# Optimization experiments

Hardware: AMD Instinct MI355X
Metric: run time of the kernel (lower is better)

The kernel has to match this reference:

```python
import jax, jax.numpy as jnp
import numpy as np

B, N, C_IN, C_OUT, H = 8, 1024, 256, 512, 8
DH = C_OUT // H  # per-head dim
LN_EPS = 1e-5


def setup_inputs() -> dict:
    key = jax.random.key(0)
    ks = jax.random.split(key, 8)
    # xavier_normal std for [in, out] fan pair
    std = float(np.sqrt(2.0 / (C_IN + DH)))
    x = jax.random.normal(ks[0], (B, N, C_IN), dtype=jnp.float32)
    adj = jax.random.uniform(ks[1], (B, N, N), dtype=jnp.float32)
    W_q = jax.random.normal(ks[2], (H, C_IN, DH), dtype=jnp.float32) * std
    W_k = jax.random.normal(ks[3], (H, C_IN, DH), dtype=jnp.float32) * std
    W_v = jax.random.normal(ks[4], (H, C_IN, DH), dtype=jnp.float32) * std
    # Conv1d(in, out, kernel=1) == pointwise linear: weight [out, in], bias [out]
    bound = float(1.0 / np.sqrt(C_IN))
    conv_w = jax.random.uniform(ks[5], (C_OUT, C_IN), dtype=jnp.float32, minval=-bound, maxval=bound)
    conv_b = jax.random.uniform(ks[6], (C_OUT,), dtype=jnp.float32, minval=-bound, maxval=bound)
    ln_w = jnp.ones((C_OUT,), dtype=jnp.float32)
    ln_b = jnp.zeros((C_OUT,), dtype=jnp.float32)
    return {"x": x, "adj": adj, "W_q": W_q, "W_k": W_k, "W_v": W_v,
            "conv_w": conv_w, "conv_b": conv_b, "ln_w": ln_w, "ln_b": ln_b}


def reference(x, adj, W_q, W_k, W_v, conv_w, conv_b, ln_w, ln_b):
    # NOTE: in the original module, adj is used only to compute D_neg/A_hat,
    # which are discarded; it has no effect on the output. Attention is dense.
    dh = W_q.shape[-1]
    scale = 1.0 / jnp.sqrt(jnp.asarray(dh, dtype=x.dtype))
    # batched per-head projections: [B,N,Cin] x [H,Cin,dh] -> [B,H,N,dh]
    Q = jnp.einsum('bni,hio->bhno', x, W_q)
    K = jnp.einsum('bni,hio->bhno', x, W_k)
    V = jnp.einsum('bni,hio->bhno', x, W_v)
    scores = jnp.einsum('bhqd,bhkd->bhqk', Q, K) * scale  # [B,H,N,N]
    attn = jax.nn.softmax(scores, axis=-1)
    out = jax.nn.relu(jnp.einsum('bhqk,bhkd->bhqd', attn, V))  # [B,H,N,dh]
    b, h, n, d = out.shape
    out = out.transpose(0, 2, 1, 3).reshape(b, n, h * d)  # concat heads -> [B,N,Cout]
    # matching_conv: 1x1 conv == linear over channels
    proj = jnp.einsum('bni,oi->bno', x, conv_w) + conv_b
    y = out + proj
    mean = jnp.mean(y, axis=-1, keepdims=True)
    var = jnp.var(y, axis=-1, keepdims=True)
    y = (y - mean) * jax.lax.rsqrt(var + LN_EPS)
    return y * ln_w + ln_b
```

## Files before the change

### kernel.cpp

```cpp
#include <hip/hip_runtime.h>

#define B_ 8
#define N_ 1024
#define CIN_ 256
#define COUT_ 512
#define H_ 8
#define DH_ 64

typedef __attribute__((ext_vector_type(8))) short bf8;
typedef __attribute__((ext_vector_type(4))) short s4;
typedef __attribute__((ext_vector_type(4))) float f4;
typedef __attribute__((ext_vector_type(2))) unsigned int u2;

__device__ __forceinline__ short f2bf(float f) {
  unsigned u = __builtin_bit_cast(unsigned, f);
  u += 0x7fffu + ((u >> 16) & 1u);
  return (short)(u >> 16);
}
__device__ __forceinline__ float bf2f(short s) {
  unsigned u = ((unsigned)(unsigned short)s) << 16;
  return __builtin_bit_cast(float, u);
}

#if __has_builtin(__builtin_amdgcn_exp2f)
#define EXP2 __builtin_amdgcn_exp2f
#else
#define EXP2 exp2f
#endif

__device__ __forceinline__ unsigned cvtpk(float a, float b) {
  unsigned u;
  asm("v_cvt_pk_bf16_f32 %0, %1, %2" : "=v"(u) : "v"(a), "v"(b));
  return u;
}

#define MFMA16(a, b, c) __builtin_amdgcn_mfma_f32_16x16x32_bf16((a), (b), (c), 0, 0, 0)

#define MFMAPV(a, b, c) __builtin_amdgcn_mfma_f32_16x16x16bf16_1k((a), (b), (c), 0, 0, 0)

#define GLD16(gp, lp)                                                              \
  __builtin_amdgcn_global_load_lds((const __attribute__((address_space(1))) void*)(gp), \
                                   (__attribute__((address_space(3))) void*)(lp), 16, 0, 0)

__global__ void k_prep(const float* __restrict__ Wq, const float* __restrict__ Wk,
                       const float* __restrict__ Wv, const float* __restrict__ Cw,
                       const float* __restrict__ x, short* __restrict__ Wt,
                       short* __restrict__ xb) {
  int blk = blockIdx.x;
  if (blk < 2048) {
    int col = blk;
    int k = threadIdx.x;
    float v;
    if (col < 512) {
      int h = col >> 6, d = col & 63;
      v = Wq[(h * CIN_ + k) * DH_ + d];
    } else if (col < 1024) {
      int c = col - 512, h = c >> 6, d = c & 63;
      v = Wk[(h * CIN_ + k) * DH_ + d];
    } else if (col < 1536) {
      int c = col - 1024, h = c >> 6, d = c & 63;
      v = Wv[(h * CIN_ + k) * DH_ + d];
    } else {
      v = Cw[(col - 1536) * CIN_ + k];
    }
    Wt[col * CIN_ + k] = f2bf(v);
  } else {
    int i = (blk - 2048) * 256 + threadIdx.x;
    f4 a = *reinterpret_cast<const f4*>(x + (size_t)i * 8);
    f4 b = *reinterpret_cast<const f4*>(x + (size_t)i * 8 + 4);
    bf8 o;
    o[0] = f2bf(a[0]); o[1] = f2bf(a[1]); o[2] = f2bf(a[2]); o[3] = f2bf(a[3]);
    o[4] = f2bf(b[0]); o[5] = f2bf(b[1]); o[6] = f2bf(b[2]); o[7] = f2bf(b[3]);
    *reinterpret_cast<bf8*>(xb + (size_t)i * 8) = o;
  }
}

__global__ __launch_bounds__(256) void k_gemm(const short* __restrict__ xb, const short* __restrict__ Wt,
                                              short* __restrict__ Qw, short* __restrict__ Kw,
                                              short* __restrict__ Vt, short* __restrict__ Pj) {
  __shared__ short Al[2][128][64];
  __shared__ short Bl[2][128][64];
  int tid = threadIdx.x;
  int mt = blockIdx.x >> 4, nt = blockIdx.x & 15;
  int row0 = mt * 128, col0 = nt * 128;
  int w = tid >> 6, lane = tid & 63, g = lane >> 4, lr = lane & 15;
  int wm = w >> 1, wn = w & 1;
  f4 acc[4][4];
#pragma unroll
  for (int i = 0; i < 4; ++i)
#pragma unroll
    for (int j = 0; j < 4; ++j) acc[i][j] = (f4){0.f, 0.f, 0.f, 0.f};

  int srow[4], sgc[4];
#pragma unroll
  for (int p = 0; p < 4; ++p) {
    int s = p * 256 + tid;
    srow[p] = s >> 3;
    sgc[p] = (s & 7) ^ (srow[p] & 7);
  }

#define STAGE_AB(k0_, buf_)                                                     \
  {                                                                             \
    char* abase = (char*)&Al[buf_][0][0];                                       \
    char* bbase = (char*)&Bl[buf_][0][0];                                       \
    _Pragma("unroll")                                                           \
    for (int p = 0; p < 4; ++p) {                                               \
      int lb = (p * 256 + w * 64) << 4;                                         \
      GLD16(xb + (row0 + srow[p]) * CIN_ + (k0_) + sgc[p] * 8, abase + lb);     \
      GLD16(Wt + (col0 + srow[p]) * CIN_ + (k0_) + sgc[p] * 8, bbase + lb);     \
    }                                                                           \
  }

  STAGE_AB(0, 0);

  for (int kt = 0; kt < 4; ++kt) {
    int cur = kt & 1;
    if (kt < 3) {
      STAGE_AB((kt + 1) * 64, cur ^ 1);
      asm volatile("s_waitcnt vmcnt(8)" ::: "memory");
    } else {
      asm volatile("s_waitcnt vmcnt(0)" ::: "memory");
    }
    __builtin_amdgcn_s_barrier();

    const short* al = &Al[cur][0][0];
    const short* bl = &Bl[cur][0][0];
    bf8 af[4][2], bb[4][2];
#pragma unroll
    for (int mi = 0; mi < 4; ++mi) {
      int R = wm * 64 + mi * 16 + lr;
      int sw = R & 7;
      af[mi][0] = *reinterpret_cast<const bf8*>(al + R * 64 + ((g ^ sw) * 8));
      af[mi][1] = *reinterpret_cast<const bf8*>(al + R * 64 + (((4 + g) ^ sw) * 8));
    }
#pragma unroll
    for (int ni = 0; ni < 4; ++ni) {
      int R = wn * 64 + ni * 16 + lr;
      int sw = R & 7;
      bb[ni][0] = *reinterpret_cast<const bf8*>(bl + R * 64 + ((g ^ sw) * 8));
      bb[ni][1] = *reinterpret_cast<const bf8*>(bl + R * 64 + (((4 + g) ^ sw) * 8));
    }
#pragma unroll
    for (int mi = 0; mi < 4; ++mi)
#pragma unroll
      for (int ni = 0; ni < 4; ++ni) {
        acc[mi][ni] = MFMA16(af[mi][0], bb[ni][0], acc[mi][ni]);
        acc[mi][ni] = MFMA16(af[mi][1], bb[ni][1], acc[mi][ni]);
      }
    asm volatile("s_waitcnt lgkmcnt(0)" ::: "memory");
    __builtin_amdgcn_s_barrier();
  }

  const float QSCL = 0.125f * 1.4426950408889634f;
#pragma unroll
  for (int mi = 0; mi < 4; ++mi)
#pragma unroll
    for (int ni = 0; ni < 4; ++ni) {
      int c = col0 + wn * 64 + ni * 16 + lr;
      int r0 = row0 + wm * 64 + mi * 16 + g * 4;
      int b = r0 >> 10, n0 = r0 & 1023;
      if (c < 1024) {
#pragma unroll
        for (int j = 0; j < 4; ++j) {
          int n = n0 + j;
          if (c < 512) {
            Qw[((b * H_ + (c >> 6)) * N_ + n) * DH_ + (c & 63)] = f2bf(acc[mi][ni][j] * QSCL);
          } else {
            int cc = c - 512;
            Kw[((b * H_ + (cc >> 6)) * N_ + n) * DH_ + (cc & 63)] = f2bf(acc[mi][ni][j]);
          }
        }
      } else if (c < 1536) {
        int cc = c - 1024;
        int hh = cc >> 6, d = cc & 63;
        s4 vv;
#pragma unroll
        for (int j = 0; j < 4; ++j) vv[j] = f2bf(acc[mi][ni][j]);
        *reinterpret_cast<s4*>(Vt + ((size_t)(b * H_ + hh) * DH_ + d) * N_ + n0) = vv;
      } else {
#pragma unroll
        for (int j = 0; j < 4; ++j) {
          Pj[(size_t)(r0 + j) * COUT_ + (c - 1536)] = f2bf(acc[mi][ni][j]);
        }
      }
    }
}

__global__ __launch_bounds__(256) void k_attn(const short* __restrict__ Qw, const short* __restrict__ Kw,
                                              const short* __restrict__ Vt, short* __restrict__ At) {
  __shared__ short Kl[4][64][64];
  __shared__ short Vl[4][64][64];
  int tid = threadIdx.x;
  int nid = ((blockIdx.x & 7) << 6) | (blockIdx.x >> 3);
  int bh = nid >> 3;
  int qb = nid & 7;
  int w = tid >> 6, lane = tid & 63, g = lane >> 4, lr = lane & 15;
  int qglob = qb * 128 + w * 32;
  const short* Qp = Qw + ((size_t)bh * N_ + qglob) * DH_;
  const short* Kp = Kw + (size_t)bh * N_ * DH_;
  const short* Vp = Vt + (size_t)bh * DH_ * N_;

  int sr0 = tid >> 3, sc0 = (tid & 7) ^ (sr0 & 7);
  int s1 = tid + 256;
  int sr1 = s1 >> 3, sc1 = (s1 & 7) ^ (sr1 & 7);
  int lo0 = (w * 64) << 4;
  int lo1 = (w * 64 + 256) << 4;

#define STAGE_KV(tt_, buf_)                                                     \
  {                                                                             \
    const short* kb = Kp + (tt_) * (64 * DH_);                                  \
    const short* vb = Vp + (tt_) * 64;                                          \
    char* klb = (char*)&Kl[buf_][0][0];                                         \
    char* vlb = (char*)&Vl[buf_][0][0];                                         \
    GLD16(kb + sr0 * 64 + sc0 * 8, klb + lo0);                                  \
    GLD16(kb + sr1 * 64 + sc1 * 8, klb + lo1);                                  \
    GLD16(vb + (size_t)sr0 * N_ + sc0 * 8, vlb + lo0);                          \
    GLD16(vb + (size_t)sr1 * N_ + sc1 * 8, vlb + lo1);                          \
  }

  STAGE_KV(0, 0);
  STAGE_KV(1, 1);

  bf8 aq[2][2];
#pragma unroll
  for (int qs = 0; qs < 2; ++qs) {
    aq[qs][0] = *reinterpret_cast<const bf8*>(Qp + (qs * 16 + lr) * DH_ + g * 8);
    aq[qs][1] = *reinterpret_cast<const bf8*>(Qp + (qs * 16 + lr) * DH_ + 32 + g * 8);
  }

  f4 o[2][4];
  f4 lacc[2];
#pragma unroll
  for (int qs = 0; qs < 2; ++qs) {
    lacc[qs] = (f4){0.f, 0.f, 0.f, 0.f};
#pragma unroll
    for (int i = 0; i < 4; ++i) o[qs][i] = (f4){0.f, 0.f, 0.f, 0.f};
  }

  for (int t = 0; t < 16; ++t) {
    int cur = t & 3;
    if (t < 14) {
      STAGE_KV(t + 2, (t + 2) & 3);
      asm volatile("s_waitcnt vmcnt(8)" ::: "memory");
    } else if (t == 14) {
      asm volatile("s_waitcnt vmcnt(4)" ::: "memory");
    } else {
      asm volatile("s_waitcnt vmcnt(0)" ::: "memory");
    }
    __builtin_amdgcn_s_barrier();

    const short* klc = &Kl[cur][0][0];
    bf8 bk0[4], bk1[4];
#pragma unroll
    for (int kt = 0; kt < 4; ++kt) {
      int R = kt * 16 + lr;
      const short* kr = klc + R * 64;
      int sw = (R & 7) << 3;
      bk0[kt] = *reinterpret_cast<const bf8*>(kr + ((g * 8) ^ sw));
      bk1[kt] = *reinterpret_cast<const bf8*>(kr + ((32 + g * 8) ^ sw));
    }
    f4 s0[4], s1v[4];
    __builtin_amdgcn_s_setprio(1);
#pragma unroll
    for (int kt = 0; kt < 4; ++kt) {
      f4 z = (f4){0.f, 0.f, 0.f, 0.f};
      z = MFMA16(bk0[kt], aq[0][0], z);
      z = MFMA16(bk1[kt], aq[0][1], z);
      s0[kt] = z;
      f4 z2 = (f4){0.f, 0.f, 0.f, 0.f};
      z2 = MFMA16(bk0[kt], aq[1][0], z2);
      z2 = MFMA16(bk1[kt], aq[1][1], z2);
      s1v[kt] = z2;
    }
    __builtin_amdgcn_s_setprio(0);
    s4 pq0[4], pq1[4];
#pragma unroll
    for (int kt = 0; kt < 4; ++kt) {
      f4 p;
      p[0] = EXP2(s0[kt][0]); p[1] = EXP2(s0[kt][1]);
      p[2] = EXP2(s0[kt][2]); p[3] = EXP2(s0[kt][3]);
      lacc[0] += p;
      u2 pk;
      pk[0] = cvtpk(p[0], p[1]);
      pk[1] = cvtpk(p[2], p[3]);
      pq0[kt] = __builtin_bit_cast(s4, pk);
    }
#pragma unroll
    for (int kt = 0; kt < 4; ++kt) {
      f4 p;
      p[0] = EXP2(s1v[kt][0]); p[1] = EXP2(s1v[kt][1]);
      p[2] = EXP2(s1v[kt][2]); p[3] = EXP2(s1v[kt][3]);
      lacc[1] += p;
      u2 pk;
      pk[0] = cvtpk(p[0], p[1]);
      pk[1] = cvtpk(p[2], p[3]);
      pq1[kt] = __builtin_bit_cast(s4, pk);
    }

    const short* vlc = &Vl[cur][0][0];
#pragma unroll
    for (int dt = 0; dt < 4; ++dt) {
      int R = dt * 16 + lr;
      const short* vr = vlc + R * 64;
      int swR = R & 7;
      s4 va[4];
#pragma unroll
      for (int kt = 0; kt < 4; ++kt) {
        int ch = (kt * 2 + (g >> 1)) ^ swR;
        va[kt] = *reinterpret_cast<const s4*>(vr + ch * 8 + (g & 1) * 4);
      }
      __builtin_amdgcn_s_setprio(1);
#pragma unroll
      for (int kt = 0; kt < 4; ++kt) {
        o[0][dt] = MFMAPV(va[kt], pq0[kt], o[0][dt]);
        o[1][dt] = MFMAPV(va[kt], pq1[kt], o[1][dt]);
      }
      __builtin_amdgcn_s_setprio(0);
    }
    asm volatile("s_waitcnt lgkmcnt(0)" ::: "memory");
  }

  float ls[2];
#pragma unroll
  for (int qs = 0; qs < 2; ++qs) {
    float v = (lacc[qs][0] + lacc[qs][1]) + (lacc[qs][2] + lacc[qs][3]);
    v += __shfl_xor(v, 16, 64);
    v += __shfl_xor(v, 32, 64);
    ls[qs] = v;
  }
  int b = bh >> 3, h = bh & 7;
#pragma unroll
  for (int qs = 0; qs < 2; ++qs) {
    float inv = 1.f / ls[qs];
    int n = qglob + qs * 16 + lr;
    short* dst = At + ((size_t)b * N_ + n) * COUT_ + h * DH_;
#pragma unroll
    for (int dt = 0; dt < 4; ++dt) {
      s4 ov;
#pragma unroll
      for (int j = 0; j < 4; ++j) ov[j] = f2bf(fmaxf(o[qs][dt][j] * inv, 0.f));
      *reinterpret_cast<s4*>(dst + dt * 16 + g * 4) = ov;
    }
  }
}

__global__ __launch_bounds__(256) void k_ln(const short* __restrict__ At, const short* __restrict__ Pj,
                                            const float* __restrict__ cb, const float* __restrict__ lw,
                                            const float* __restrict__ lb, float* __restrict__ out) {
  int row = blockIdx.x * 4 + (threadIdx.x >> 6);
  int lane = threadIdx.x & 63;
  int c0 = lane * 8;
  bf8 a8 = *reinterpret_cast<const bf8*>(At + (size_t)row * COUT_ + c0);
  bf8 p8 = *reinterpret_cast<const bf8*>(Pj + (size_t)row * COUT_ + c0);
  float y[8];
  float sum = 0.f, sq = 0.f;
#pragma unroll
  for (int j = 0; j < 8; ++j) {
    float v = bf2f(a8[j]) + bf2f(p8[j]) + cb[c0 + j];
    y[j] = v;
    sum += v;
    sq += v * v;
  }
#pragma unroll
  for (int off = 1; off < 64; off <<= 1) {
    sum += __shfl_xor(sum, off, 64);
    sq += __shfl_xor(sq, off, 64);
  }
  float mean = sum * (1.f / 512.f);
  float var = sq * (1.f / 512.f) - mean * mean;
  float rstd = rsqrtf(var + 1e-5f);
  f4 o0, o1;
#pragma unroll
  for (int j = 0; j < 4; ++j) o0[j] = (y[j] - mean) * rstd * lw[c0 + j] + lb[c0 + j];
#pragma unroll
  for (int j = 0; j < 4; ++j) o1[j] = (y[4 + j] - mean) * rstd * lw[c0 + 4 + j] + lb[c0 + 4 + j];
  *reinterpret_cast<f4*>(out + (size_t)row * COUT_ + c0) = o0;
  *reinterpret_cast<f4*>(out + (size_t)row * COUT_ + c0 + 4) = o1;
}

extern "C" void kernel_launch(void* const* d_in, const int* in_sizes, int n_in,
                              void* d_out, int out_size, void* d_ws, size_t ws_size,
                              hipStream_t stream) {
  const float* x  = (const float*)d_in[0];
  const float* Wq = (const float*)d_in[2];
  const float* Wk = (const float*)d_in[3];
  const float* Wv = (const float*)d_in[4];
  const float* Cw = (const float*)d_in[5];
  const float* cb = (const float*)d_in[6];
  const float* lw = (const float*)d_in[7];
  const float* lb = (const float*)d_in[8];
  float* out = (float*)d_out;
  char* ws = (char*)d_ws;
  short* xb = (short*)(ws);
  short* Wt = (short*)(ws + (size_t)4194304);
  short* Qw = (short*)(ws + (size_t)5242880);
  short* Kw = (short*)(ws + (size_t)13631488);
  short* Vt = (short*)(ws + (size_t)22020096);
  short* Pj = (short*)(ws + (size_t)30408704);
  short* At = (short*)(ws + (size_t)38797312);

  hipLaunchKernelGGL(k_prep, dim3(3072), dim3(256), 0, stream, Wq, Wk, Wv, Cw, x, Wt, xb);
  hipLaunchKernelGGL(k_gemm, dim3(1024), dim3(256), 0, stream, xb, Wt, Qw, Kw, Vt, Pj);
  hipLaunchKernelGGL(k_attn, dim3(512), dim3(256), 0, stream, Qw, Kw, Vt, At);
  hipLaunchKernelGGL(k_ln, dim3(2048), dim3(256), 0, stream, At, Pj, cb, lw, lb, out);
}
```

Baseline: 66.40 us.

## Store Q transposed and fold projection residual add into attention epilogue

The GEMM epilogue now writes Q in a head-dim-major transposed layout with vectorized 4-element stores, like V, instead of scattered scalar stores. The attention kernel gathers Q with strided scalar loads before staging K/V. It also adds the bf16 projection result into the attention output before storing it. The layernorm kernel then reads only one bf16 tensor instead of two. The change cuts GEMM store scatter and LN read traffic, but adds uncoalesced Q loads in attention and an extra rounding of the summed value to bf16.

```diff
diff --git a/kernel.cpp b/kernel.cpp
--- a/kernel.cpp
+++ b/kernel.cpp
@@ -35,7 +35,6 @@
 }
 
 #define MFMA16(a, b, c) __builtin_amdgcn_mfma_f32_16x16x32_bf16((a), (b), (c), 0, 0, 0)
-
 #define MFMAPV(a, b, c) __builtin_amdgcn_mfma_f32_16x16x16bf16_1k((a), (b), (c), 0, 0, 0)
 
 #define GLD16(gp, lp)                                                              \
@@ -76,7 +75,7 @@
 }
 
 __global__ __launch_bounds__(256) void k_gemm(const short* __restrict__ xb, const short* __restrict__ Wt,
-                                              short* __restrict__ Qw, short* __restrict__ Kw,
+                                              short* __restrict__ Qt, short* __restrict__ Kw,
                                               short* __restrict__ Vt, short* __restrict__ Pj) {
   __shared__ short Al[2][128][64];
   __shared__ short Bl[2][128][64];
@@ -159,16 +158,18 @@
       int c = col0 + wn * 64 + ni * 16 + lr;
       int r0 = row0 + wm * 64 + mi * 16 + g * 4;
       int b = r0 >> 10, n0 = r0 & 1023;
-      if (c < 1024) {
+      if (c < 512) {
+        int hh = c >> 6, d = c & 63;
+        s4 vv;
+#pragma unroll
+        for (int j = 0; j < 4; ++j) vv[j] = f2bf(acc[mi][ni][j] * QSCL);
+        *reinterpret_cast<s4*>(Qt + ((size_t)(b * H_ + hh) * DH_ + d) * N_ + n0) = vv;
+      } else if (c < 1024) {
+        int cc = c - 512;
 #pragma unroll
         for (int j = 0; j < 4; ++j) {
           int n = n0 + j;
-          if (c < 512) {
-            Qw[((b * H_ + (c >> 6)) * N_ + n) * DH_ + (c & 63)] = f2bf(acc[mi][ni][j] * QSCL);
-          } else {
-            int cc = c - 512;
-            Kw[((b * H_ + (cc >> 6)) * N_ + n) * DH_ + (cc & 63)] = f2bf(acc[mi][ni][j]);
-          }
+          Kw[((b * H_ + (cc >> 6)) * N_ + n) * DH_ + (cc & 63)] = f2bf(acc[mi][ni][j]);
         }
       } else if (c < 1536) {
         int cc = c - 1024;
@@ -186,8 +187,9 @@
     }
 }
 
-__global__ __launch_bounds__(256) void k_attn(const short* __restrict__ Qw, const short* __restrict__ Kw,
-                                              const short* __restrict__ Vt, short* __restrict__ At) {
+__global__ __launch_bounds__(256) void k_attn(const short* __restrict__ Qt, const short* __restrict__ Kw,
+                                              const short* __restrict__ Vt, const short* __restrict__ Pj,
+                                              short* __restrict__ At) {
   __shared__ short Kl[4][64][64];
   __shared__ short Vl[4][64][64];
   int tid = threadIdx.x;
@@ -196,9 +198,20 @@
   int qb = nid & 7;
   int w = tid >> 6, lane = tid & 63, g = lane >> 4, lr = lane & 15;
   int qglob = qb * 128 + w * 32;
-  const short* Qp = Qw + ((size_t)bh * N_ + qglob) * DH_;
+  const short* Qp = Qt + (size_t)bh * DH_ * N_;
   const short* Kp = Kw + (size_t)bh * N_ * DH_;
   const short* Vp = Vt + (size_t)bh * DH_ * N_;
+
+  bf8 aq[2][2];
+#pragma unroll
+  for (int qs = 0; qs < 2; ++qs) {
+    int n = qglob + qs * 16 + lr;
+#pragma unroll
+    for (int e = 0; e < 8; ++e) {
+      aq[qs][0][e] = Qp[(size_t)(g * 8 + e) * N_ + n];
+      aq[qs][1][e] = Qp[(size_t)(32 + g * 8 + e) * N_ + n];
+    }
+  }
 
   int sr0 = tid >> 3, sc0 = (tid & 7) ^ (sr0 & 7);
   int s1 = tid + 256;
@@ -221,13 +234,6 @@
   STAGE_KV(0, 0);
   STAGE_KV(1, 1);
 
-  bf8 aq[2][2];
-#pragma unroll
-  for (int qs = 0; qs < 2; ++qs) {
-    aq[qs][0] = *reinterpret_cast<const bf8*>(Qp + (qs * 16 + lr) * DH_ + g * 8);
-    aq[qs][1] = *reinterpret_cast<const bf8*>(Qp + (qs * 16 + lr) * DH_ + 32 + g * 8);
-  }
-
   f4 o[2][4];
   f4 lacc[2];
 #pragma unroll
@@ -333,30 +339,32 @@
   for (int qs = 0; qs < 2; ++qs) {
     float inv = 1.f / ls[qs];
     int n = qglob + qs * 16 + lr;
+    const short* pr = Pj + ((size_t)b * N_ + n) * COUT_ + h * DH_;
     short* dst = At + ((size_t)b * N_ + n) * COUT_ + h * DH_;
 #pragma unroll
     for (int dt = 0; dt < 4; ++dt) {
+      s4 pj4 = *reinterpret_cast<const s4*>(pr + dt * 16 + g * 4);
       s4 ov;
 #pragma unroll
-      for (int j = 0; j < 4; ++j) ov[j] = f2bf(fmaxf(o[qs][dt][j] * inv, 0.f));
+      for (int j = 0; j < 4; ++j)
+        ov[j] = f2bf(fmaxf(o[qs][dt][j] * inv, 0.f) + bf2f(pj4[j]));
       *reinterpret_cast<s4*>(dst + dt * 16 + g * 4) = ov;
     }
   }
 }
 
-__global__ __launch_bounds__(256) void k_ln(const short* __restrict__ At, const short* __restrict__ Pj,
+__global__ __launch_bounds__(256) void k_ln(const short* __restrict__ At,
                                             const float* __restrict__ cb, const float* __restrict__ lw,
                                             const float* __restrict__ lb, float* __restrict__ out) {
   int row = blockIdx.x * 4 + (threadIdx.x >> 6);
   int lane = threadIdx.x & 63;
   int c0 = lane * 8;
   bf8 a8 = *reinterpret_cast<const bf8*>(At + (size_t)row * COUT_ + c0);
-  bf8 p8 = *reinterpret_cast<const bf8*>(Pj + (size_t)row * COUT_ + c0);
   float y[8];
   float sum = 0.f, sq = 0.f;
 #pragma unroll
   for (int j = 0; j < 8; ++j) {
-    float v = bf2f(a8[j]) + bf2f(p8[j]) + cb[c0 + j];
+    float v = bf2f(a8[j]) + cb[c0 + j];
     y[j] = v;
     sum += v;
     sq += v * v;
@@ -393,14 +401,14 @@
   char* ws = (char*)d_ws;
   short* xb = (short*)(ws);
   short* Wt = (short*)(ws + (size_t)4194304);
-  short* Qw = (short*)(ws + (size_t)5242880);
+  short* Qt = (short*)(ws + (size_t)5242880);
   short* Kw = (short*)(ws + (size_t)13631488);
   short* Vt = (short*)(ws + (size_t)22020096);
   short* Pj = (short*)(ws + (size_t)30408704);
   short* At = (short*)(ws + (size_t)38797312);
 
   hipLaunchKernelGGL(k_prep, dim3(3072), dim3(256), 0, stream, Wq, Wk, Wv, Cw, x, Wt, xb);
-  hipLaunchKernelGGL(k_gemm, dim3(1024), dim3(256), 0, stream, xb, Wt, Qw, Kw, Vt, Pj);
-  hipLaunchKernelGGL(k_attn, dim3(512), dim3(256), 0, stream, Qw, Kw, Vt, At);
-  hipLaunchKernelGGL(k_ln, dim3(2048), dim3(256), 0, stream, At, Pj, cb, lw, lb, out);
-}
+  hipLaunchKernelGGL(k_gemm, dim3(1024), dim3(256), 0, stream, xb, Wt, Qt, Kw, Vt, Pj);
+  hipLaunchKernelGGL(k_attn, dim3(512), dim3(256), 0, stream, Qt, Kw, Vt, Pj, At);
+  hipLaunchKernelGGL(k_ln, dim3(2048), dim3(256), 0, stream, At, cb, lw, lb, out);
+}
```

Measured after the change: 65.94 us. Within noise of the previous version (-0.7%).
